# Optimization experiments

Hardware: AMD Instinct MI355X
Metric: run time of the kernel (lower is better)

Reference implementation:

```python
import jax, jax.numpy as jnp
import numpy as np

H = 4  # num heads, hard-coded in Encoder's GAT(hidden, hidden, hidden, 4, 2)


def build_adjacency(shot_type, encode_length):
    # Faithful vectorized port of initialize_adjacency_matrix.
    B, S = shot_type.shape
    N = 2 * encode_length
    base = np.zeros((14, N, N), dtype=np.int32)
    base[13] = 1 - np.eye(N, dtype=np.int32)  # complete graph minus self-loops
    for row in range(N):
        ni = row // 2
        if row % 2 == 0:
            col = (ni + 1) * 2
            rel = 11 if ni % 2 == 0 else 12
        else:
            col = (ni + 1) * 2 + 1
            rel = 12 if ni % 2 == 0 else 11
        if col <= N - 1:
            base[rel, row, col] = 1
            base[rel, col, row] = 1
            base[13, row, col] = 0
            base[13, col, row] = 0
    adj = jnp.tile(jnp.asarray(base)[None], (B, 1, 1, 1))  # [B,14,N,N]
    steps = np.arange(S)
    even = steps % 2 == 0
    i = np.where(even, 2 * steps, 2 * steps + 1)
    j = np.where(even, 2 * (steps + 1) + 1, 2 * (steps + 1))
    b = np.broadcast_to(np.arange(B)[:, None], (B, S))
    i = np.broadcast_to(i, (B, S))
    j = np.broadcast_to(j, (B, S))
    adj = adj.at[b, shot_type, i, j].set(1)
    adj = adj.at[b, shot_type, j, i].set(1)
    adj = adj.at[b, 13, i, j].set(0)
    adj = adj.at[b, 13, j, i].set(0)
    return adj


def gat_layer(x, mask, W, att):
    # x: [B,N,in], W: [in, H*F], att: [H, 2F]; standard GAT concat-score,
    # computed as a_src.h_i + a_dst.h_j (== a^T [h_i || h_j]).
    B, N, _ = x.shape
    F = att.shape[1] // 2
    h = (x @ W).reshape(B, N, H, F).transpose(0, 2, 1, 3)       # [B,H,N,F]
    s_src = jnp.einsum('bhnf,hf->bhn', h, att[:, :F])
    s_dst = jnp.einsum('bhnf,hf->bhn', h, att[:, F:])
    scores = s_src[:, :, :, None] + s_dst[:, :, None, :]        # [B,H,N,N]
    scores = jnp.where(scores > 0, scores, 0.2 * scores)        # LeakyReLU(0.2)
    scores = jnp.where(mask[:, None], scores, -jnp.inf)
    attn = jax.nn.softmax(scores, axis=-1)                      # dropout: eval mode
    hp = jnp.einsum('bhij,bhjf->bhif', attn, h)
    return hp.transpose(0, 2, 1, 3).reshape(B, N, H * F)


def setup_inputs() -> dict:
    B, E = 32, 256
    player_num, player_dim, location_dim, hidden = 35, 32, 32, 64
    k = jax.random.split(jax.random.key(0), 16)

    def lin(key, fan_in, shape):
        return jax.random.normal(key, shape, dtype=jnp.float32) / np.sqrt(fan_in)

    return {
        'player': jax.random.randint(k[0], (B, 2), 0, player_num),
        'shot_type': jax.random.randint(k[1], (B, E - 1), 0, 11),
        'player_A_x': jax.random.uniform(k[2], (B, E), dtype=jnp.float32),
        'player_A_y': jax.random.uniform(k[3], (B, E), dtype=jnp.float32),
        'player_B_x': jax.random.uniform(k[4], (B, E), dtype=jnp.float32),
        'player_B_y': jax.random.uniform(k[5], (B, E), dtype=jnp.float32),
        'encode_length': E,
        'emb_table': jax.random.normal(k[6], (player_num, player_dim), dtype=jnp.float32),
        'Wc': lin(k[7], 2, (2, location_dim)),
        'bc': jnp.zeros((location_dim,), dtype=jnp.float32),
        'Wm': lin(k[8], player_dim + location_dim, (player_dim + location_dim, hidden)),
        'bm': jnp.zeros((hidden,), dtype=jnp.float32),
        'lin1_W': lin(k[9], hidden, (hidden, H * hidden)),
        'att1': lin(k[10], 2 * hidden, (H, 2 * hidden)),
        'lin2_W': lin(k[11], H * hidden, (H * hidden, H * hidden)),
        'att2': lin(k[12], 2 * hidden, (H, 2 * hidden)),
    }


def reference(player, shot_type, player_A_x, player_A_y, player_B_x, player_B_y,
              encode_length, emb_table, Wc, bc, Wm, bm, lin1_W, att1, lin2_W, att2):
    E = int(encode_length)
    B = player.shape[0]
    adj = build_adjacency(shot_type, E)                 # [B,14,N,N]
    mask = adj.sum(axis=1) > 0                          # union over relations [B,N,N]
    coord_A = jnp.stack([player_A_x, player_A_y], axis=-1)   # [B,E,2]
    coord_B = jnp.stack([player_B_x, player_B_y], axis=-1)
    coord = jnp.stack([coord_A, coord_B], axis=2).reshape(B, -1, 2)  # [B,2E,2]
    ct = jax.nn.relu(coord @ Wc + bc)                   # [B,2E,loc]
    p = jnp.tile(player, (1, E))                        # [B,2E]
    pe = emb_table[p]                                   # [B,2E,pdim]
    x = jnp.concatenate([ct, pe], axis=-1) @ Wm + bm    # [B,2E,hidden]
    x = jax.nn.relu(gat_layer(x, mask, lin1_W, att1))
    node_embedding = gat_layer(x, mask, lin2_W, att2)   # [B,2E,H*hidden]
    return node_embedding, adj
```

## Files before the change

### kernel.cpp

```cpp
#include <hip/hip_runtime.h>
#include <hip/hip_bf16.h>
#include <stdint.h>

static constexpr int B_  = 32;
static constexpr int E_  = 256;
static constexpr int N_  = 512;
static constexpr int C_  = 256;
static constexpr int BN  = B_ * N_;
static constexpr int NODE_ELEMS = B_ * N_ * C_;
static constexpr int ADJ_ELEMS  = B_ * 14 * N_ * N_;

#define LOG2E 1.44269504088896340736f

typedef __attribute__((ext_vector_type(8))) short v8bf;
typedef __attribute__((ext_vector_type(4))) float v4f;

__device__ __forceinline__ unsigned short f2bfbits(float f) {
  union { float f; unsigned u; } x; x.f = f;
  unsigned u = x.u;
  return (unsigned short)((u + 0x7FFFu + ((u >> 16) & 1u)) >> 16);
}

struct ConvArgs {
  const void* src[15];
  void* dst[15];
  int n[15];
  int kind[15];
};

__global__ __launch_bounds__(256) void k_conv2(ConvArgs a, const unsigned* fprobe,
                                               const unsigned* iprobe) {
  __shared__ int fk_s, ik_s;
  int t = threadIdx.x;
  if (t == 0) {
    int c_even = 0, c_lo = 0;
    for (int k = 0; k < 32; ++k) {
      unsigned w = fprobe[2 * k];
      unsigned e32 = (w >> 23) & 0xFFu;
      unsigned elo = (w >> 7) & 0xFFu;
      if (e32 >= 105u && e32 <= 135u) ++c_even;
      if (elo >= 105u && elo <= 135u) ++c_lo;
    }
    fk_s = (c_even < 16) ? 2 : ((c_lo >= 16) ? 1 : 0);
    int hi0 = 0;
    for (int k = 0; k < 32; ++k) if (iprobe[2 * k + 1] == 0u) ++hi0;
    ik_s = (hi0 >= 30) ? 1 : 0;
  }
  __syncthreads();
  int fk = fk_s, ik = ik_s;
  int arr = blockIdx.y;
  int n = a.n[arr], kind = a.kind[arr];
  for (int idx = blockIdx.x * 256 + t; idx < n; idx += gridDim.x * 256) {
    if (kind == 1) {
      int v;
      if (ik == 1) v = (int)((const long long*)a.src[arr])[idx];
      else         v = ((const int*)a.src[arr])[idx];
      ((int*)a.dst[arr])[idx] = v;
    } else {
      float v;
      if (fk == 2) {
        v = (float)((const double*)a.src[arr])[idx];
      } else if (fk == 1) {
        unsigned short u = ((const unsigned short*)a.src[arr])[idx];
        union { unsigned u; float f; } c; c.u = (unsigned)u << 16; v = c.f;
      } else {
        v = ((const float*)a.src[arr])[idx];
      }
      if (kind == 0) {
        ((float*)a.dst[arr])[idx] = v;
      } else {
        int kk = idx >> 8, cc = idx & 255;
        ((unsigned short*)a.dst[arr])[cc * 256 + kk] = f2bfbits(v);
      }
    }
  }
}

__global__ __launch_bounds__(256) void k_feat4(
    const int* __restrict__ player, const float* __restrict__ Ax, const float* __restrict__ Ay,
    const float* __restrict__ Bx, const float* __restrict__ By,
    const float* __restrict__ emb, const float* __restrict__ Wc, const float* __restrict__ bc,
    const float* __restrict__ Wm, const float* __restrict__ bm, float* __restrict__ x) {
  int t = threadIdx.x, sub = t >> 6, lane = t & 63;
  int id = blockIdx.x * 4 + sub;
  int b = id >> 9, n = id & 511;
  int e = n >> 1, side = n & 1;
  __shared__ float feat[4][64];
  float v;
  if (lane < 32) {
    float cx = side ? Bx[b * E_ + e] : Ax[b * E_ + e];
    float cy = side ? By[b * E_ + e] : Ay[b * E_ + e];
    v = fmaxf(fmaf(cx, Wc[lane], fmaf(cy, Wc[32 + lane], bc[lane])), 0.f);
  } else {
    int pid = player[b * 2 + side];
    v = emb[pid * 32 + (lane - 32)];
  }
  feat[sub][lane] = v;
  __syncthreads();
  float acc = bm[lane];
  #pragma unroll 8
  for (int c = 0; c < 64; ++c) acc = fmaf(feat[sub][c], Wm[c * 64 + lane], acc);
  x[(size_t)id * 64 + lane] = acc;
}

__global__ __launch_bounds__(256) void k_gemm(
    const float* __restrict__ x, const float* __restrict__ W, float* __restrict__ h, int K,
    const float* __restrict__ att, float* __restrict__ ssO, float* __restrict__ sdO) {
  __shared__ float xs[64 * 64];
  __shared__ float wt[64 * 64];
  int row0 = blockIdx.x * 64;
  int col0 = blockIdx.y * 64;
  int hd = blockIdx.y;
  int t = threadIdx.x;
  int tx = t & 15, ty = t >> 4;
  float acc[4][4] = {};
  for (int kt = 0; kt < K; kt += 64) {
    #pragma unroll
    for (int q = 0; q < 4; ++q) {
      int v = q * 256 + t;
      int r = v >> 4, c = (v & 15) * 4;
      *(float4*)&xs[r * 64 + c] = *(const float4*)&x[(size_t)(row0 + r) * K + kt + c];
      *(float4*)&wt[r * 64 + c] = *(const float4*)&W[(size_t)(kt + r) * C_ + col0 + c];
    }
    __syncthreads();
    #pragma unroll 4
    for (int k = 0; k < 64; ++k) {
      float xv[4];
      #pragma unroll
      for (int r = 0; r < 4; ++r) xv[r] = xs[(ty * 4 + r) * 64 + k];
      float4 wf = *(const float4*)&wt[k * 64 + tx * 4];
      #pragma unroll
      for (int r = 0; r < 4; ++r) {
        acc[r][0] = fmaf(xv[r], wf.x, acc[r][0]);
        acc[r][1] = fmaf(xv[r], wf.y, acc[r][1]);
        acc[r][2] = fmaf(xv[r], wf.z, acc[r][2]);
        acc[r][3] = fmaf(xv[r], wf.w, acc[r][3]);
      }
    }
    __syncthreads();
  }
  #pragma unroll
  for (int r = 0; r < 4; ++r) {
    int row = row0 + ty * 4 + r;
    float4 o = make_float4(acc[r][0], acc[r][1], acc[r][2], acc[r][3]);
    *(float4*)&h[(size_t)row * C_ + col0 + tx * 4] = o;
  }
  float attS[4], attD[4];
  #pragma unroll
  for (int c = 0; c < 4; ++c) {
    attS[c] = att[hd * 128 + tx * 4 + c];
    attD[c] = att[hd * 128 + 64 + tx * 4 + c];
  }
  #pragma unroll
  for (int r = 0; r < 4; ++r) {
    float p1 = acc[r][0] * attS[0] + acc[r][1] * attS[1] + acc[r][2] * attS[2] + acc[r][3] * attS[3];
    float p2 = acc[r][0] * attD[0] + acc[r][1] * attD[1] + acc[r][2] * attD[2] + acc[r][3] * attD[3];
    #pragma unroll
    for (int d = 8; d > 0; d >>= 1) {
      p1 += __shfl_xor(p1, d, 16);
      p2 += __shfl_xor(p2, d, 16);
    }
    if (tx == 0) {
      int row = row0 + ty * 4 + r;
      int bb = row >> 9, nn = row & 511;
      int idx = (bb * 4 + hd) * N_ + nn;
      ssO[idx] = p1; sdO[idx] = p2;
    }
  }
}

__global__ __launch_bounds__(256) void k_gemm2_mfma(
    const unsigned short* __restrict__ xb, const unsigned short* __restrict__ wt,
    float* __restrict__ h, const float* __restrict__ att,
    float* __restrict__ ssO, float* __restrict__ sdO) {
  int row0 = blockIdx.x * 64;
  int col0 = blockIdx.y * 64;
  int hd = blockIdx.y;
  int t = threadIdx.x, w = t >> 6, l = t & 63;
  int lane16 = l & 15, quad = l >> 4;
  int arow = row0 + w * 16 + lane16;
  v4f acc[4] = {};
  #pragma unroll
  for (int ks = 0; ks < 8; ++ks) {
    int kb = ks * 32 + quad * 8;
    v8bf a = *(const v8bf*)&xb[(size_t)arow * 256 + kb];
    #pragma unroll
    for (int fs = 0; fs < 4; ++fs) {
      v8bf b = *(const v8bf*)&wt[(size_t)(col0 + fs * 16 + lane16) * 256 + kb];
      acc[fs] = __builtin_amdgcn_mfma_f32_16x16x32_bf16(a, b, acc[fs], 0, 0, 0);
    }
  }
  float attS[4], attD[4];
  #pragma unroll
  for (int fs = 0; fs < 4; ++fs) {
    attS[fs] = att[hd * 128 + fs * 16 + lane16];
    attD[fs] = att[hd * 128 + 64 + fs * 16 + lane16];
  }
  #pragma unroll
  for (int r = 0; r < 4; ++r) {
    int row = row0 + w * 16 + quad * 4 + r;
    #pragma unroll
    for (int fs = 0; fs < 4; ++fs)
      h[(size_t)row * C_ + col0 + fs * 16 + lane16] = acc[fs][r];
    float p1 = acc[0][r] * attS[0] + acc[1][r] * attS[1] + acc[2][r] * attS[2] + acc[3][r] * attS[3];
    float p2 = acc[0][r] * attD[0] + acc[1][r] * attD[1] + acc[2][r] * attD[2] + acc[3][r] * attD[3];
    #pragma unroll
    for (int d = 8; d > 0; d >>= 1) {
      p1 += __shfl_xor(p1, d, 16);
      p2 += __shfl_xor(p2, d, 16);
    }
    if (lane16 == 0) {
      int bb = row >> 9, nn = row & 511;
      int idx = (bb * 4 + hd) * N_ + nn;
      ssO[idx] = p1; sdO[idx] = p2;
    }
  }
}

template <int RELU>
__global__ __launch_bounds__(256) void k_attn_mfma3(
    const float* __restrict__ h, const float* __restrict__ ss, const float* __restrict__ sd,
    void* __restrict__ outp) {
  __shared__ unsigned short hs[64 * 74];
  __shared__ float sdl[512];
  __shared__ float red[4];
  __shared__ float ls[4][16];
  int blk = blockIdx.x;
  int it = blk & 7, hd = (blk >> 3) & 3, b = blk >> 5;
  int i0 = it * 64, bh = b * 4 + hd;
  int t = threadIdx.x, w = t >> 6, l = t & 63;
  int lane16 = l & 15, quad = l >> 4;
  float v0 = sd[(size_t)bh * N_ + t];
  float v1 = sd[(size_t)bh * N_ + 256 + t];
  sdl[t] = v0; sdl[256 + t] = v1;
  float mx = fmaxf(v0, v1);
  #pragma unroll
  for (int d = 32; d > 0; d >>= 1) mx = fmaxf(mx, __shfl_xor(mx, d, 64));
  if (l == 0) red[w] = mx;
  __syncthreads();
  mx = fmaxf(fmaxf(red[0], red[1]), fmaxf(red[2], red[3]));
  int iw = i0 + w * 16 + lane16;
  float ss_s = ss[(size_t)bh * N_ + iw];
  float sv0 = ss_s + mx;
  float m2_s = fmaxf(sv0, 0.2f * sv0) * LOG2E;
  float lsum = 0.f;
  v4f acc[4] = {};
  for (int jt = 0; jt < 8; ++jt) {
    int j0 = jt * 64;
    #pragma unroll
    for (int q = 0; q < 4; ++q) {
      int v = q * 256 + t;
      int j = v >> 4, f0 = (v & 15) * 4;
      float4 hv = *(const float4*)&h[(size_t)(b * N_ + j0 + j) * C_ + hd * 64 + f0];
      hs[(f0 + 0) * 74 + j] = f2bfbits(hv.x);
      hs[(f0 + 1) * 74 + j] = f2bfbits(hv.y);
      hs[(f0 + 2) * 74 + j] = f2bfbits(hv.z);
      hs[(f0 + 3) * 74 + j] = f2bfbits(hv.w);
    }
    __syncthreads();
    #pragma unroll
    for (int ks = 0; ks < 2; ++ks) {
      int kb = ks * 32;
      v8bf afr;
      #pragma unroll
      for (int q = 0; q < 8; ++q) {
        int j = j0 + kb + quad * 8 + q;
        float sv = ss_s + sdl[j];
        float sc = fmaxf(sv, 0.2f * sv);
        float p = exp2f(fmaf(sc, LOG2E, -m2_s));
        if (iw == j) p = 0.f;
        lsum += p;
        afr[q] = (short)f2bfbits(p);
      }
      #pragma unroll
      for (int fs = 0; fs < 4; ++fs) {
        v8bf bfr = *(const v8bf*)&hs[(fs * 16 + lane16) * 74 + kb + quad * 8];
        acc[fs] = __builtin_amdgcn_mfma_f32_16x16x32_bf16(afr, bfr, acc[fs], 0, 0, 0);
      }
    }
    __syncthreads();
  }
  lsum += __shfl_xor(lsum, 16, 64);
  lsum += __shfl_xor(lsum, 32, 64);
  if (quad == 0) ls[w][lane16] = lsum;
  __syncthreads();
  #pragma unroll
  for (int r = 0; r < 4; ++r) {
    int i = i0 + w * 16 + quad * 4 + r;
    float scale = 1.f / ls[w][quad * 4 + r];
    #pragma unroll
    for (int fs = 0; fs < 4; ++fs) {
      int f = fs * 16 + lane16;
      float vv = acc[fs][r] * scale;
      size_t o = (size_t)(b * N_ + i) * C_ + hd * 64 + f;
      if constexpr (RELU) {
        ((unsigned short*)outp)[o] = f2bfbits(fmaxf(vv, 0.f));
      } else {
        ((float*)outp)[o] = vv;
      }
    }
  }
}

__global__ __launch_bounds__(256) void k_adjf3(
    const int* __restrict__ st, float* __restrict__ adj) {
  int plane = blockIdx.y;
  int r = plane % 14;
  int b = plane / 14;
  int i0 = blockIdx.x * 8;
  const int* stb = st + b * 255;
  size_t base = (size_t)plane * (512 * 512);
  #pragma unroll
  for (int itr = 0; itr < 4; ++itr) {
    int lin = itr * 256 + threadIdx.x;
    int i = i0 + (lin >> 7);
    int j0 = (lin & 127) << 2;
    float vals[4];
    #pragma unroll
    for (int q = 0; q < 4; ++q) {
      int j = j0 + q;
      int d = j - i;
      int ad = d < 0 ? -d : d;
      int mn = d < 0 ? j : i;
      int m4 = mn & 3;
      float v = 0.f;
      if (r == 13) {
        bool excl = (d == 0) || (ad == 2) || (ad == 3 && m4 == 0) || (ad == 1 && m4 == 3);
        v = excl ? 0.f : 1.f;
      } else if (r == 11) {
        v = (ad == 2 && (m4 == 0 || m4 == 3)) ? 1.f : 0.f;
      } else if (r == 12) {
        v = (ad == 2 && (m4 == 1 || m4 == 2)) ? 1.f : 0.f;
      } else {
        bool sp = (ad == 3 && m4 == 0) || (ad == 1 && m4 == 3);
        if (sp) v = (stb[mn >> 1] == r) ? 1.f : 0.f;
      }
      vals[q] = v;
    }
    v4f o = { vals[0], vals[1], vals[2], vals[3] };
    __builtin_nontemporal_store(o, (v4f*)&adj[base + (size_t)i * 512 + j0]);
  }
}

__global__ __launch_bounds__(256) void k_adjf(
    const unsigned* __restrict__ st_raw, float* __restrict__ adj) {
  __shared__ int i64_s;
  if (threadIdx.x == 0) {
    int hi0 = 0;
    for (int k = 0; k < 32; ++k) if (st_raw[2 * k + 1] == 0u) ++hi0;
    i64_s = (hi0 >= 30) ? 1 : 0;
  }
  __syncthreads();
  int is64 = i64_s;
  int chunk = blockIdx.x * 256 + threadIdx.x;
  int j0 = (chunk & 127) << 2;
  int rowid = chunk >> 7;
  int i = rowid & 511;
  int plane = rowid >> 9;
  int r = plane % 14;
  int b = plane / 14;
  float vals[4];
  #pragma unroll
  for (int q = 0; q < 4; ++q) {
    int j = j0 + q;
    int d = j - i;
    int ad = d < 0 ? -d : d;
    int mn = d < 0 ? j : i;
    int m4 = mn & 3;
    float v = 0.f;
    if (r == 13) {
      bool excl = (d == 0) || (ad == 2) || (ad == 3 && m4 == 0) || (ad == 1 && m4 == 3);
      v = excl ? 0.f : 1.f;
    } else if (r == 11) {
      v = (ad == 2 && (m4 == 0 || m4 == 3)) ? 1.f : 0.f;
    } else if (r == 12) {
      v = (ad == 2 && (m4 == 1 || m4 == 2)) ? 1.f : 0.f;
    } else {
      bool sp = (ad == 3 && m4 == 0) || (ad == 1 && m4 == 3);
      if (sp) {
        int e = b * 255 + (mn >> 1);
        int stv = is64 ? (int)st_raw[2 * e] : (int)st_raw[e];
        v = (stv == r) ? 1.f : 0.f;
      }
    }
    vals[q] = v;
  }
  *(float4*)&adj[(size_t)chunk * 4] = make_float4(vals[0], vals[1], vals[2], vals[3]);
}

__global__ void k_sentinel(float* out, float v) {
  if (threadIdx.x == 0 && blockIdx.x == 0) out[0] = v;
}

extern "C" void kernel_launch(void* const* d_in, const int* in_sizes, int n_in,
                              void* d_out, int out_size, void* d_ws, size_t ws_size,
                              hipStream_t stream) {
  static const int expA[16] = {64,8160,8192,8192,8192,8192,1,1120,64,32,4096,64,16384,512,65536,512};
  static const int expB[15] = {64,8160,8192,8192,8192,8192,1120,64,32,4096,64,16384,512,65536,512};
  int mismatch = -1;
  int base = 7;
  if (n_in == 16) {
    base = 7;
    for (int i = 0; i < 16; ++i) if (in_sizes[i] != expA[i]) { mismatch = i; break; }
  } else if (n_in == 15) {
    base = 6;
    for (int i = 0; i < 15; ++i) if (in_sizes[i] != expB[i]) { mismatch = i; break; }
  } else {
    mismatch = 17;
  }
  if (mismatch < 0 && out_size != NODE_ELEMS + ADJ_ELEMS) mismatch = 16;

  float* out_node = (float*)d_out;
  float* out_adjf = out_node + NODE_ELEMS;

  char* scr = (char*)out_adjf;
  float* x  = (float*)(scr);
  float* h  = (float*)(scr + (size_t)( 4u << 20));
  unsigned short* x2b = (unsigned short*)(scr + (size_t)(24u << 20));
  float* ss = (float*)(scr + (size_t)(44u << 20));
  float* sd = (float*)(scr + (size_t)(45u << 20));
  float* cv = (float*)(scr + (size_t)(48u << 20));

  float* cAx  = cv + 0;
  float* cAy  = cv + 8192;
  float* cBx  = cv + 16384;
  float* cBy  = cv + 24576;
  float* cEmb = cv + 32768;
  float* cWc  = cv + 33888;
  float* cbc  = cv + 33952;
  float* cWm  = cv + 33984;
  float* cbm  = cv + 38080;
  float* cW1  = cv + 38144;
  float* cA1  = cv + 54528;
  unsigned short* cW2T = (unsigned short*)(cv + 55040);
  float* cA2  = cv + 120576;
  int*   cPl  = (int*)(cv + 121088);

  bool ws_ok = (ws_size >= 8160 * sizeof(int));
  int* cSt = ws_ok ? (int*)d_ws : nullptr;

  ConvArgs a;
  a.src[0]  = d_in[2];        a.dst[0]  = cAx;  a.n[0]  = 8192;  a.kind[0]  = 0;
  a.src[1]  = d_in[3];        a.dst[1]  = cAy;  a.n[1]  = 8192;  a.kind[1]  = 0;
  a.src[2]  = d_in[4];        a.dst[2]  = cBx;  a.n[2]  = 8192;  a.kind[2]  = 0;
  a.src[3]  = d_in[5];        a.dst[3]  = cBy;  a.n[3]  = 8192;  a.kind[3]  = 0;
  a.src[4]  = d_in[base + 0]; a.dst[4]  = cEmb; a.n[4]  = 1120;  a.kind[4]  = 0;
  a.src[5]  = d_in[base + 1]; a.dst[5]  = cWc;  a.n[5]  = 64;    a.kind[5]  = 0;
  a.src[6]  = d_in[base + 2]; a.dst[6]  = cbc;  a.n[6]  = 32;    a.kind[6]  = 0;
  a.src[7]  = d_in[base + 3]; a.dst[7]  = cWm;  a.n[7]  = 4096;  a.kind[7]  = 0;
  a.src[8]  = d_in[base + 4]; a.dst[8]  = cbm;  a.n[8]  = 64;    a.kind[8]  = 0;
  a.src[9]  = d_in[base + 5]; a.dst[9]  = cW1;  a.n[9]  = 16384; a.kind[9]  = 0;
  a.src[10] = d_in[base + 6]; a.dst[10] = cA1;  a.n[10] = 512;   a.kind[10] = 0;
  a.src[11] = d_in[base + 7]; a.dst[11] = cW2T; a.n[11] = 65536; a.kind[11] = 2;
  a.src[12] = d_in[base + 8]; a.dst[12] = cA2;  a.n[12] = 512;   a.kind[12] = 0;
  a.src[13] = d_in[0];        a.dst[13] = cPl;  a.n[13] = 64;    a.kind[13] = 1;
  a.src[14] = d_in[1];        a.dst[14] = ws_ok ? (void*)cSt : (void*)cPl;
  a.n[14] = ws_ok ? 8160 : 0; a.kind[14] = 1;

  k_conv2<<<dim3(64, 15), 256, 0, stream>>>(a, (const unsigned*)d_in[base + 3],
                                            (const unsigned*)d_in[0]);

  k_feat4<<<BN / 4, 256, 0, stream>>>(cPl, cAx, cAy, cBx, cBy, cEmb, cWc, cbc, cWm, cbm, x);

  k_gemm<<<dim3(BN / 64, 4), 256, 0, stream>>>(x, cW1, h, 64, cA1, ss, sd);
  k_attn_mfma3<1><<<B_ * 4 * (N_ / 64), 256, 0, stream>>>(h, ss, sd, x2b);

  k_gemm2_mfma<<<dim3(BN / 64, 4), 256, 0, stream>>>(x2b, cW2T, h, cA2, ss, sd);
  k_attn_mfma3<0><<<B_ * 4 * (N_ / 64), 256, 0, stream>>>(h, ss, sd, out_node);

  if (ws_ok) {
    k_adjf3<<<dim3(64, 448), 256, 0, stream>>>(cSt, out_adjf);
  } else {
    k_adjf<<<(ADJ_ELEMS / 4) / 256, 256, 0, stream>>>((const unsigned*)d_in[1], out_adjf);
  }

  if (mismatch >= 0) {
    float v = ldexpf(1024.f, mismatch);
    k_sentinel<<<1, 64, 0, stream>>>(out_node, v);
  }
}
```

Baseline: 616.3 us.

## Store projected features as transposed bf16 so attention reads MFMA fragments directly

The GEMM kernels now write the projected features h as bf16 in a feature-major (transposed) layout rather than row-major fp32. The attention kernel can then load MFMA B-fragments straight from global memory, dropping the LDS staging, the per-tile fp32-to-bf16 conversion and the two barriers per tile. The row-sum exchange moves from LDS to a lane shuffle, and the final fp32 output store becomes nontemporal. This halves the bytes of h written and read and removes synchronisation. The cost is strided global stores in the GEMM epilogue and uncached direct fragment loads in attention, which depend on L2 reuse across blocks.

```diff
diff --git a/kernel.cpp b/kernel.cpp
--- a/kernel.cpp
+++ b/kernel.cpp
@@ -104,8 +104,8 @@
 }
 
 __global__ __launch_bounds__(256) void k_gemm(
-    const float* __restrict__ x, const float* __restrict__ W, float* __restrict__ h, int K,
-    const float* __restrict__ att, float* __restrict__ ssO, float* __restrict__ sdO) {
+    const float* __restrict__ x, const float* __restrict__ W, unsigned short* __restrict__ hbT,
+    int K, const float* __restrict__ att, float* __restrict__ ssO, float* __restrict__ sdO) {
   __shared__ float xs[64 * 64];
   __shared__ float wt[64 * 64];
   int row0 = blockIdx.x * 64;
@@ -140,10 +140,12 @@
     __syncthreads();
   }
   #pragma unroll
-  for (int r = 0; r < 4; ++r) {
-    int row = row0 + ty * 4 + r;
-    float4 o = make_float4(acc[r][0], acc[r][1], acc[r][2], acc[r][3]);
-    *(float4*)&h[(size_t)row * C_ + col0 + tx * 4] = o;
+  for (int c = 0; c < 4; ++c) {
+    unsigned f = (unsigned)(col0 + tx * 4 + c);
+    ushort4 o;
+    o.x = f2bfbits(acc[0][c]); o.y = f2bfbits(acc[1][c]);
+    o.z = f2bfbits(acc[2][c]); o.w = f2bfbits(acc[3][c]);
+    *(ushort4*)&hbT[(f << 14) + row0 + ty * 4] = o;
   }
   float attS[4], attD[4];
   #pragma unroll
@@ -171,7 +173,7 @@
 
 __global__ __launch_bounds__(256) void k_gemm2_mfma(
     const unsigned short* __restrict__ xb, const unsigned short* __restrict__ wt,
-    float* __restrict__ h, const float* __restrict__ att,
+    unsigned short* __restrict__ hbT, const float* __restrict__ att,
     float* __restrict__ ssO, float* __restrict__ sdO) {
   int row0 = blockIdx.x * 64;
   int col0 = blockIdx.y * 64;
@@ -190,6 +192,14 @@
       acc[fs] = __builtin_amdgcn_mfma_f32_16x16x32_bf16(a, b, acc[fs], 0, 0, 0);
     }
   }
+  #pragma unroll
+  for (int fs = 0; fs < 4; ++fs) {
+    unsigned f = (unsigned)(col0 + fs * 16 + lane16);
+    ushort4 o;
+    o.x = f2bfbits(acc[fs][0]); o.y = f2bfbits(acc[fs][1]);
+    o.z = f2bfbits(acc[fs][2]); o.w = f2bfbits(acc[fs][3]);
+    *(ushort4*)&hbT[(f << 14) + row0 + w * 16 + quad * 4] = o;
+  }
   float attS[4], attD[4];
   #pragma unroll
   for (int fs = 0; fs < 4; ++fs) {
@@ -199,9 +209,6 @@
   #pragma unroll
   for (int r = 0; r < 4; ++r) {
     int row = row0 + w * 16 + quad * 4 + r;
-    #pragma unroll
-    for (int fs = 0; fs < 4; ++fs)
-      h[(size_t)row * C_ + col0 + fs * 16 + lane16] = acc[fs][r];
     float p1 = acc[0][r] * attS[0] + acc[1][r] * attS[1] + acc[2][r] * attS[2] + acc[3][r] * attS[3];
     float p2 = acc[0][r] * attD[0] + acc[1][r] * attD[1] + acc[2][r] * attD[2] + acc[3][r] * attD[3];
     #pragma unroll
@@ -218,13 +225,11 @@
 }
 
 template <int RELU>
-__global__ __launch_bounds__(256) void k_attn_mfma3(
-    const float* __restrict__ h, const float* __restrict__ ss, const float* __restrict__ sd,
-    void* __restrict__ outp) {
-  __shared__ unsigned short hs[64 * 74];
+__global__ __launch_bounds__(256) void k_attn_mfma4(
+    const unsigned short* __restrict__ hbT, const float* __restrict__ ss,
+    const float* __restrict__ sd, void* __restrict__ outp) {
   __shared__ float sdl[512];
   __shared__ float red[4];
-  __shared__ float ls[4][16];
   int blk = blockIdx.x;
   int it = blk & 7, hd = (blk >> 3) & 3, b = blk >> 5;
   int i0 = it * 64, bh = b * 4 + hd;
@@ -245,26 +250,16 @@
   float m2_s = fmaxf(sv0, 0.2f * sv0) * LOG2E;
   float lsum = 0.f;
   v4f acc[4] = {};
+  const unsigned short* hb = hbT + ((unsigned)(hd * 64) << 14) + b * 512;
   for (int jt = 0; jt < 8; ++jt) {
     int j0 = jt * 64;
     #pragma unroll
-    for (int q = 0; q < 4; ++q) {
-      int v = q * 256 + t;
-      int j = v >> 4, f0 = (v & 15) * 4;
-      float4 hv = *(const float4*)&h[(size_t)(b * N_ + j0 + j) * C_ + hd * 64 + f0];
-      hs[(f0 + 0) * 74 + j] = f2bfbits(hv.x);
-      hs[(f0 + 1) * 74 + j] = f2bfbits(hv.y);
-      hs[(f0 + 2) * 74 + j] = f2bfbits(hv.z);
-      hs[(f0 + 3) * 74 + j] = f2bfbits(hv.w);
-    }
-    __syncthreads();
-    #pragma unroll
     for (int ks = 0; ks < 2; ++ks) {
-      int kb = ks * 32;
+      int kb = ks * 32 + quad * 8;
       v8bf afr;
       #pragma unroll
       for (int q = 0; q < 8; ++q) {
-        int j = j0 + kb + quad * 8 + q;
+        int j = j0 + kb + q;
         float sv = ss_s + sdl[j];
         float sc = fmaxf(sv, 0.2f * sv);
         float p = exp2f(fmaf(sc, LOG2E, -m2_s));
@@ -274,20 +269,17 @@
       }
       #pragma unroll
       for (int fs = 0; fs < 4; ++fs) {
-        v8bf bfr = *(const v8bf*)&hs[(fs * 16 + lane16) * 74 + kb + quad * 8];
+        v8bf bfr = *(const v8bf*)&hb[((unsigned)(fs * 16 + lane16) << 14) + j0 + kb];
         acc[fs] = __builtin_amdgcn_mfma_f32_16x16x32_bf16(afr, bfr, acc[fs], 0, 0, 0);
       }
     }
-    __syncthreads();
   }
   lsum += __shfl_xor(lsum, 16, 64);
   lsum += __shfl_xor(lsum, 32, 64);
-  if (quad == 0) ls[w][lane16] = lsum;
-  __syncthreads();
   #pragma unroll
   for (int r = 0; r < 4; ++r) {
     int i = i0 + w * 16 + quad * 4 + r;
-    float scale = 1.f / ls[w][quad * 4 + r];
+    float scale = 1.f / __shfl(lsum, quad * 4 + r, 16);
     #pragma unroll
     for (int fs = 0; fs < 4; ++fs) {
       int f = fs * 16 + lane16;
@@ -296,7 +288,7 @@
       if constexpr (RELU) {
         ((unsigned short*)outp)[o] = f2bfbits(fmaxf(vv, 0.f));
       } else {
-        ((float*)outp)[o] = vv;
+        __builtin_nontemporal_store(vv, &((float*)outp)[o]);
       }
     }
   }
@@ -415,7 +407,7 @@
 
   char* scr = (char*)out_adjf;
   float* x  = (float*)(scr);
-  float* h  = (float*)(scr + (size_t)( 4u << 20));
+  unsigned short* hbT = (unsigned short*)(scr + (size_t)( 4u << 20));
   unsigned short* x2b = (unsigned short*)(scr + (size_t)(24u << 20));
   float* ss = (float*)(scr + (size_t)(44u << 20));
   float* sd = (float*)(scr + (size_t)(45u << 20));
@@ -462,11 +454,11 @@
 
   k_feat4<<<BN / 4, 256, 0, stream>>>(cPl, cAx, cAy, cBx, cBy, cEmb, cWc, cbc, cWm, cbm, x);
 
-  k_gemm<<<dim3(BN / 64, 4), 256, 0, stream>>>(x, cW1, h, 64, cA1, ss, sd);
-  k_attn_mfma3<1><<<B_ * 4 * (N_ / 64), 256, 0, stream>>>(h, ss, sd, x2b);
-
-  k_gemm2_mfma<<<dim3(BN / 64, 4), 256, 0, stream>>>(x2b, cW2T, h, cA2, ss, sd);
-  k_attn_mfma3<0><<<B_ * 4 * (N_ / 64), 256, 0, stream>>>(h, ss, sd, out_node);
+  k_gemm<<<dim3(BN / 64, 4), 256, 0, stream>>>(x, cW1, hbT, 64, cA1, ss, sd);
+  k_attn_mfma4<1><<<B_ * 4 * (N_ / 64), 256, 0, stream>>>(hbT, ss, sd, x2b);
+
+  k_gemm2_mfma<<<dim3(BN / 64, 4), 256, 0, stream>>>(x2b, cW2T, hbT, cA2, ss, sd);
+  k_attn_mfma4<0><<<B_ * 4 * (N_ / 64), 256, 0, stream>>>(hbT, ss, sd, out_node);
 
   if (ws_ok) {
     k_adjf3<<<dim3(64, 448), 256, 0, stream>>>(cSt, out_adjf);
```

Result: no change. 622.7 us (+1.0%).
